# Performance work log

Measured on AMD Instinct MI355X. Metric: run time of the kernel, lower is better.

Reference implementation:

```python
import jax, jax.numpy as jnp
import numpy as np

NH = 8          # attention heads
TEMP = 2.0      # gumbel temperature


def _gumbel_softmax_hard(logits, key, temperature):
    # hard=True straight-through gumbel softmax (module is in eval mode)
    g = jax.random.gumbel(key, logits.shape, logits.dtype)
    y = jax.nn.softmax((logits + g) / temperature, axis=-1)
    y_hard = jax.nn.one_hot(jnp.argmax(y, axis=-1), logits.shape[-1], dtype=y.dtype)
    return y_hard - jax.lax.stop_gradient(y) + y


def _experts(x, w1, w2, w3):
    # SwiGLU FFN over all experts at once: x [T,C], w1/w3 [E,H,C], w2 [E,C,H] -> [T,E,C]
    h = jax.nn.silu(jnp.einsum('tc,ehc->teh', x, w1)) * jnp.einsum('tc,ehc->teh', x, w3)
    return jnp.einsum('teh,ech->tec', h, w2)


def _mha(q_in, kv_in, in_w, in_b, out_w, out_b):
    C = q_in.shape[-1]
    hd = C // NH
    q = q_in @ in_w[:C].T + in_b[:C]
    k = kv_in @ in_w[C:2 * C].T + in_b[C:2 * C]
    v = kv_in @ in_w[2 * C:].T + in_b[2 * C:]
    B, Tq, _ = q.shape
    Tk = k.shape[1]
    q = q.reshape(B, Tq, NH, hd)
    k = k.reshape(B, Tk, NH, hd)
    v = v.reshape(B, Tk, NH, hd)
    scale = jnp.asarray(1.0 / np.sqrt(hd), q.dtype)
    att = jax.nn.softmax(jnp.einsum('bqhd,bkhd->bhqk', q, k) * scale, axis=-1)
    o = jnp.einsum('bhqk,bkhd->bqhd', att, v).reshape(B, Tq, C)
    return o @ out_w.T + out_b


def setup_inputs() -> dict:
    key = jax.random.key(0)
    ks = jax.random.split(key, 20)
    B, T, S, C, E, H = 2, 2048, 77, 1024, 4, 2816
    p = lambda k, sh: jax.random.normal(k, sh, jnp.float32) * 0.02
    return {
        'x': jax.random.normal(ks[0], (B, T, C), jnp.float32),
        'time': jax.random.normal(ks[1], (B,), jnp.float32),
        'caption': jax.random.normal(ks[2], (B, S, C), jnp.float32),
        'language': jax.random.randint(ks[3], (B,), 0, 9),
        'lang_embed': p(ks[4], (9, C)),
        'lang_gate_w': p(ks[5], (E, C)),
        'lang_gate_b': jnp.zeros((E,), jnp.float32),
        'lang_w1': p(ks[6], (E, H, C)),
        'lang_w2': p(ks[7], (E, C, H)),
        'lang_w3': p(ks[8], (E, H, C)),
        'in_proj_w': p(ks[9], (3 * C, C)),
        'in_proj_b': jnp.zeros((3 * C,), jnp.float32),
        'out_proj_w': p(ks[10], (C, C)),
        'out_proj_b': jnp.zeros((C,), jnp.float32),
        'cap_gate_w': p(ks[11], (E, C)),
        'cap_gate_b': jnp.zeros((E,), jnp.float32),
        'cap_w1': p(ks[12], (E, H, C)),
        'cap_w2': p(ks[13], (E, C, H)),
        'cap_w3': p(ks[14], (E, H, C)),
    }


def reference(x, time, caption, language, lang_embed, lang_gate_w, lang_gate_b,
              lang_w1, lang_w2, lang_w3, in_proj_w, in_proj_b, out_proj_w, out_proj_b,
              cap_gate_w, cap_gate_b, cap_w1, cap_w2, cap_w3):
    B, T, C = x.shape
    x_flat = x.reshape(-1, C)                                   # [B*T, C]

    # language gating (one logit vector per batch element, repeated over T tokens)
    lang_emb = lang_embed[language]                             # [B, C]
    lang_logits = lang_emb @ lang_gate_w.T + lang_gate_b        # [B, E]
    lang_probs = _gumbel_softmax_hard(lang_logits, jax.random.key(1), TEMP)
    lang_probs = jnp.repeat(lang_probs, T, axis=0)              # [B*T, E]

    lang_outputs = _experts(x_flat, lang_w1, lang_w2, lang_w3)  # [B*T, E, C]
    first_out = (lang_outputs * lang_probs[:, :, None]).sum(axis=1)  # [B*T, C]
    first_reshaped = first_out.reshape(B, T, C)

    # cross attention against caption, then per-token caption gating
    cross = _mha(first_reshaped, caption, in_proj_w, in_proj_b, out_proj_w, out_proj_b)
    cross_flat = cross.reshape(-1, C)
    cap_logits = cross_flat @ cap_gate_w.T + cap_gate_b         # [B*T, E]
    cap_probs = _gumbel_softmax_hard(cap_logits, jax.random.key(2), TEMP)

    cap_outputs = _experts(first_out, cap_w1, cap_w2, cap_w3)   # [B*T, E, C]
    second_out = (cap_outputs * cap_probs[:, :, None]).sum(axis=1)

    total_out = (first_out + second_out).reshape(B, T, C)

    all_probs = jnp.concatenate([lang_probs, cap_probs], axis=1)  # [B*T, 2E]
    expert_usage = all_probs.mean(axis=0)
    loss = (expert_usage * jnp.log(expert_usage + 1e-10)).sum()
    return total_out, loss
```

## Files before the change

### kernel.cpp

```cpp
#include <hip/hip_runtime.h>
#include <stdint.h>

#define B_ 2
#define T_ 2048
#define S_ 77
#define C_ 1024
#define E_ 4
#define H_ 2816
#define NH_ 8
#define HD_ 128
#define N_ (B_*T_)
#define MAXGB (N_/128 + E_)
#define MAXGB2 (N_/256 + E_)
#define PEsz ((size_t)H_*C_)
#define CC_ ((size_t)C_*C_)

typedef _Float16 h8 __attribute__((ext_vector_type(8)));
typedef _Float16 h4 __attribute__((ext_vector_type(4)));
typedef float f4 __attribute__((ext_vector_type(4)));

__device__ __forceinline__ void gload16(const void* g, void* l){
  __builtin_amdgcn_global_load_lds((const __attribute__((address_space(1))) void*)g,
                                   (__attribute__((address_space(3))) void*)l, 16, 0, 0);
}

__device__ __forceinline__ void xcd_swizzle_cm(int& bx, int& by){
  int nx = gridDim.x, ny = gridDim.y;
  int nwg = nx*ny;
  int wg = by*nx + bx;
  int q = nwg >> 3, r = nwg & 7;
  int xcd = wg & 7, idx = wg >> 3;
  int s = (xcd < r ? xcd*(q+1) : r*(q+1) + (xcd-r)*q) + idx;
  bx = s / ny; by = s % ny;
}

__device__ __forceinline__ uint32_t rotl32(uint32_t v, int r){ return (v<<r)|(v>>(32-r)); }
__device__ __forceinline__ void threefry2x32(uint32_t k0, uint32_t k1,
                                             uint32_t x, uint32_t y,
                                             uint32_t& o0, uint32_t& o1){
  uint32_t k2 = k0 ^ k1 ^ 0x1BD11BDAu;
  x += k0; y += k1;
#define TFR(r) { x += y; y = rotl32(y, r); y ^= x; }
  TFR(13) TFR(15) TFR(26) TFR(6)   x += k1; y += k2 + 1u;
  TFR(17) TFR(29) TFR(16) TFR(24)  x += k2; y += k0 + 2u;
  TFR(13) TFR(15) TFR(26) TFR(6)   x += k0; y += k1 + 3u;
  TFR(17) TFR(29) TFR(16) TFR(24)  x += k1; y += k2 + 4u;
  TFR(13) TFR(15) TFR(26) TFR(6)   x += k2; y += k0 + 5u;
#undef TFR
  o0 = x; o1 = y;
}
__device__ __forceinline__ float gumbel_from_bits(uint32_t bits){
  const float TINY = 1.17549435e-38f;
  float f = __uint_as_float((bits >> 9) | 0x3f800000u) - 1.0f;
  float u = fmaxf(TINY, f + TINY);
  return -logf(-logf(u));
}
__device__ __forceinline__ float jax_gumbel(uint32_t k0, uint32_t k1, uint32_t idx){
  uint32_t a, b;
  threefry2x32(k0, k1, 0u, idx, a, b);
  return gumbel_from_bits(a ^ b);
}

__device__ __forceinline__ void job_split(const float* __restrict__ s,
    _Float16* __restrict__ hi, _Float16* __restrict__ lo, long n4, int b0, int nb){
  for (long i = (long)b0*256 + threadIdx.x; i < n4; i += (long)nb*256){
    float4 v = ((const float4*)s)[i];
    h4 h, L;
    h[0]=(_Float16)v.x; h[1]=(_Float16)v.y; h[2]=(_Float16)v.z; h[3]=(_Float16)v.w;
    L[0]=(_Float16)(v.x-(float)h[0]); L[1]=(_Float16)(v.y-(float)h[1]);
    L[2]=(_Float16)(v.z-(float)h[2]); L[3]=(_Float16)(v.w-(float)h[3]);
    ((h4*)hi)[i] = h; ((h4*)lo)[i] = L;
  }
}
__device__ __forceinline__ void job_plain(const float* __restrict__ s,
    _Float16* __restrict__ d, long n4, int b0, int nb){
  for (long i = (long)b0*256 + threadIdx.x; i < n4; i += (long)nb*256){
    float4 v = ((const float4*)s)[i];
    h4 h;
    h[0]=(_Float16)v.x; h[1]=(_Float16)v.y; h[2]=(_Float16)v.z; h[3]=(_Float16)v.w;
    ((h4*)d)[i] = h;
  }
}
__device__ __forceinline__ void job_w13_plain(const float* __restrict__ w1,
    const float* __restrict__ w3, _Float16* __restrict__ dst, int nslot, int b0, int nb){
  const int K8 = C_/8;
  long total = (long)nslot * (2*H_) * K8;
  for (long i = (long)b0*256 + threadIdx.x; i < total; i += (long)nb*256){
    int kv = (int)(i & (K8-1));
    long rs = i >> 7;
    int r  = (int)(rs % (2*H_));
    int slot = (int)(rs / (2*H_));
    int gg = r >> 5, o = r & 31;
    const float* src = ((o<16)? w1 : w3) + (size_t)slot*PEsz + (size_t)(16*gg + (o&15))*C_ + kv*8;
    float4 v0 = *(const float4*)src, v1 = *(const float4*)(src+4);
    float vv[8] = {v0.x,v0.y,v0.z,v0.w,v1.x,v1.y,v1.z,v1.w};
    h8 hh;
#pragma unroll
    for (int jj=0;jj<8;++jj) hh[jj] = (_Float16)vv[jj];
    *(h8*)(dst + (size_t)slot*2*PEsz + (size_t)r*C_ + kv*8) = hh;
  }
}
__device__ __forceinline__ void job_w13_split_sel(const float* __restrict__ w1,
    const float* __restrict__ w3, int sel0, int sel1,
    _Float16* __restrict__ hi, _Float16* __restrict__ lo, int b0, int nb){
  const int K8 = C_/8;
  long total = 2L * (2*H_) * K8;
  for (long i = (long)b0*256 + threadIdx.x; i < total; i += (long)nb*256){
    int kv = (int)(i & (K8-1));
    long rs = i >> 7;
    int r  = (int)(rs % (2*H_));
    int slot = (int)(rs / (2*H_));
    int e = slot ? sel1 : sel0;
    int gg = r >> 5, o = r & 31;
    const float* src = ((o<16)? w1 : w3) + (size_t)e*PEsz + (size_t)(16*gg + (o&15))*C_ + kv*8;
    float4 v0 = *(const float4*)src, v1 = *(const float4*)(src+4);
    float vv[8] = {v0.x,v0.y,v0.z,v0.w,v1.x,v1.y,v1.z,v1.w};
    h8 hh, ll;
#pragma unroll
    for (int jj=0;jj<8;++jj){
      hh[jj] = (_Float16)vv[jj];
      ll[jj] = (_Float16)(vv[jj]-(float)hh[jj]);
    }
    size_t dof = (size_t)slot*2*PEsz + (size_t)r*C_ + kv*8;
    *(h8*)(hi + dof) = hh;
    *(h8*)(lo + dof) = ll;
  }
}
__device__ __forceinline__ void job_w2_split_sel(const float* __restrict__ w2,
    int sel0, int sel1, _Float16* __restrict__ hi, _Float16* __restrict__ lo, int b0, int nb){
  long per = (long)(PEsz/4);
  for (long i = (long)b0*256 + threadIdx.x; i < 2*per; i += (long)nb*256){
    int slot = (i >= per) ? 1 : 0;
    long ii = i - (long)slot*per;
    float4 v = ((const float4*)(w2 + (size_t)(slot?sel1:sel0)*PEsz))[ii];
    h4 h, L;
    h[0]=(_Float16)v.x; h[1]=(_Float16)v.y; h[2]=(_Float16)v.z; h[3]=(_Float16)v.w;
    L[0]=(_Float16)(v.x-(float)h[0]); L[1]=(_Float16)(v.y-(float)h[1]);
    L[2]=(_Float16)(v.z-(float)h[2]); L[3]=(_Float16)(v.w-(float)h[3]);
    ((h4*)(hi + (size_t)slot*PEsz))[ii] = h;
    ((h4*)(lo + (size_t)slot*PEsz))[ii] = L;
  }
}
__device__ __forceinline__ void job_foldw(const float* __restrict__ outw,
    const float* __restrict__ capgw, const float* __restrict__ outb,
    float* __restrict__ Wp, float* __restrict__ bp, int b0){
  int e = b0 >> 2;
  int k = ((b0 & 3) << 8) + threadIdx.x;
  const float* cg = capgw + e*C_;
  float acc = 0.f;
  for (int c = 0; c < C_; ++c) acc += cg[c] * outw[(size_t)c*C_ + k];
  Wp[e*C_ + k] = acc;
  if ((b0 & 3) == 0){
    int wv = threadIdx.x >> 6, l = threadIdx.x & 63;
    const float* cg2 = capgw + wv*C_;
    float a2 = 0.f;
    for (int c = l; c < C_; c += 64) a2 += outb[c] * cg2[c];
#pragma unroll
    for (int off = 32; off; off >>= 1) a2 += __shfl_xor(a2, off);
    if (l == 0 && e == 0) bp[wv] = a2;
  }
}

#define CVA_W13 1024
#define CVA_W2  512
#define CVA_X   256
#define CVA_TOT (CVA_W13+CVA_W2+CVA_X)
__global__ __launch_bounds__(256) void convA(
    const float* __restrict__ lang_embed, const float* __restrict__ gate_w,
    const float* __restrict__ gate_b, const int* __restrict__ language,
    const float* __restrict__ w1, const float* __restrict__ w3, const float* __restrict__ w2,
    const float* __restrict__ x,
    _Float16* __restrict__ w13hi, _Float16* __restrict__ w13lo,
    _Float16* __restrict__ w2hi, _Float16* __restrict__ w2lo,
    _Float16* __restrict__ xhi, _Float16* __restrict__ xlo,
    float* __restrict__ langP, int* __restrict__ counts)
{
  __shared__ float lds8[8];
  const int tid = threadIdx.x, w = tid>>6, l = tid&63;
  for (int p = 2*w; p < 2*w+2; ++p){
    int b = p>>2, e = p&3;
    const float* emb = lang_embed + (size_t)language[b]*C_;
    const float* gw  = gate_w + (size_t)e*C_;
    float acc = 0.f;
    for (int c = l; c < C_; c += 64) acc += emb[c]*gw[c];
#pragma unroll
    for (int off = 32; off; off >>= 1) acc += __shfl_xor(acc, off);
    if (l == 0) lds8[p] = acc + gate_b[e];
  }
  __syncthreads();
  int sel[2];
  for (int b = 0; b < 2; ++b){
    float z[4], m = -3.4e38f;
    for (int e = 0; e < 4; ++e){
      float g = jax_gumbel(0u, 1u, (uint32_t)(b*4 + e));
      z[e] = (lds8[b*4 + e] + g) * 0.5f;
      m = fmaxf(m, z[e]);
    }
    float y[4], sum = 0.f;
    for (int e = 0; e < 4; ++e){ y[e] = expf(z[e]-m); sum += y[e]; }
    for (int e = 0; e < 4; ++e) y[e] = y[e] / sum;
    int best = 0; float bv = y[0];
    for (int e = 1; e < 4; ++e) if (y[e] > bv){ bv = y[e]; best = e; }
    sel[b] = best;
    if (blockIdx.x == 0 && tid == 0){
      for (int e = 0; e < 4; ++e)
        langP[b*4 + e] = ((e == best) ? 1.0f : 0.0f) - y[e] + y[e];
    }
  }
  if (blockIdx.x == 0 && tid == 0){
    for (int e = 0; e < 4; ++e) counts[e] = 0;
  }
  int bid = blockIdx.x;
  if (bid < CVA_W13)                 job_w13_split_sel(w1, w3, sel[0], sel[1], w13hi, w13lo, bid, CVA_W13);
  else if (bid < CVA_W13+CVA_W2)     job_w2_split_sel(w2, sel[0], sel[1], w2hi, w2lo, bid-CVA_W13, CVA_W2);
  else                               job_split(x, xhi, xlo, (long)((size_t)N_*C_/4), bid-CVA_W13-CVA_W2, CVA_X);
}

__global__ __launch_bounds__(512,2) void gemm_gate_split(
    const _Float16* __restrict__ Ahi, const _Float16* __restrict__ Alo,
    const _Float16* __restrict__ Bhi, const _Float16* __restrict__ Blo,
    _Float16* __restrict__ Hhi, _Float16* __restrict__ Hlo)
{
  __shared__ __align__(16) char smem[147456];
  const int tid = threadIdx.x, w = tid>>6, l = tid&63;
  const int lm = l&15, g = l>>4;
  const int wm = w>>1, wn = w&1;
  int bx = blockIdx.x, by = blockIdx.y;
  xcd_swizzle_cm(bx, by);
  const int n0 = bx<<7;
  const int m0 = by<<8;
  const size_t eoff = (m0 >= T_) ? (size_t)2*PEsz : 0;

  const _Float16* srcA[4]; const _Float16* srcB[2];
#pragma unroll
  for (int jj=0;jj<4;++jj){
    int c = jj*512 + tid, r = c>>3, s = c&7;
    int st = s ^ (r&7);
    srcA[jj] = (st<4 ? Ahi : Alo) + (size_t)(m0 + r)*C_ + ((st&3)<<3);
  }
#pragma unroll
  for (int jj=0;jj<2;++jj){
    int c = jj*512 + tid, r = c>>3, s = c&7;
    int st = s ^ (r&7);
    srcB[jj] = (st<4 ? Bhi : Blo) + eoff + (size_t)(n0 + r)*C_ + ((st&3)<<3);
  }

#define STGF(ts, bi) { \
    int k0 = (ts)<<5; \
    char* db = smem + (bi)*49152; \
    _Pragma("unroll") \
    for (int jj=0;jj<4;++jj) gload16(srcA[jj]+k0, db + (jj*512 + w*64)*16); \
    _Pragma("unroll") \
    for (int jj=0;jj<2;++jj) gload16(srcB[jj]+k0, db + 32768 + (jj*512 + w*64)*16); \
  }

  const int shi = (g ^ (lm&7)) << 4;
  int aoff[4], boff[4];
#pragma unroll
  for (int i=0;i<4;++i){
    aoff[i] = ((wm*64 + i*16 + lm)<<7) + shi;
    boff[i] = 32768 + ((wn*64 + i*16 + lm)<<7) + shi;
  }

  f4 acc[4][4] = {};
  const int nt = C_/32;
  STGF(0,0) STGF(1,1)
  for (int t=0; t<nt; ++t){
    const int bi = t%3;
    const bool ds = (t+2 < nt);
    const int k2 = (t+2)<<5;
    char* db2 = smem + ((t+2)%3)*49152;
    if (t+1 < nt) { asm volatile("s_waitcnt vmcnt(6)" ::: "memory"); }
    else          { asm volatile("s_waitcnt vmcnt(0)" ::: "memory"); }
    __builtin_amdgcn_s_barrier();
    asm volatile("" ::: "memory");
    const char* base = smem + bi*49152;
    if (ds){
      gload16(srcA[0]+k2, db2 + (0*512 + w*64)*16);
      gload16(srcA[1]+k2, db2 + (1*512 + w*64)*16);
    }
    h8 ah[4], bh[4];
#pragma unroll
    for (int i=0;i<4;++i){ ah[i] = *(const h8*)(base + aoff[i]); bh[i] = *(const h8*)(base + boff[i]); }
    __builtin_amdgcn_s_setprio(1);
#pragma unroll
    for (int mi=0;mi<4;++mi)
#pragma unroll
      for (int ni=0;ni<4;++ni)
        acc[mi][ni] = __builtin_amdgcn_mfma_f32_16x16x32_f16(ah[mi], bh[ni], acc[mi][ni],0,0,0);
    __builtin_amdgcn_s_setprio(0);
    if (ds){
      gload16(srcA[2]+k2, db2 + (2*512 + w*64)*16);
      gload16(srcA[3]+k2, db2 + (3*512 + w*64)*16);
    }
    h8 bl[4];
#pragma unroll
    for (int i=0;i<4;++i) bl[i] = *(const h8*)(base + (boff[i]^64));
    __builtin_amdgcn_s_setprio(1);
#pragma unroll
    for (int mi=0;mi<4;++mi)
#pragma unroll
      for (int ni=0;ni<4;++ni)
        acc[mi][ni] = __builtin_amdgcn_mfma_f32_16x16x32_f16(ah[mi], bl[ni], acc[mi][ni],0,0,0);
    __builtin_amdgcn_s_setprio(0);
    if (ds){
      gload16(srcB[0]+k2, db2 + 32768 + (0*512 + w*64)*16);
      gload16(srcB[1]+k2, db2 + 32768 + (1*512 + w*64)*16);
    }
    h8 al[4];
#pragma unroll
    for (int i=0;i<4;++i) al[i] = *(const h8*)(base + (aoff[i]^64));
    __builtin_amdgcn_s_setprio(1);
#pragma unroll
    for (int mi=0;mi<4;++mi)
#pragma unroll
      for (int ni=0;ni<4;++ni)
        acc[mi][ni] = __builtin_amdgcn_mfma_f32_16x16x32_f16(al[mi], bh[ni], acc[mi][ni],0,0,0);
    __builtin_amdgcn_s_setprio(0);
    asm volatile("" ::: "memory");
  }
#undef STGF

#pragma unroll
  for (int mi=0;mi<4;++mi){
#pragma unroll
    for (int p=0;p<2;++p){
      int hc = ((n0 + wn*64)>>1) + p*16 + lm;
#pragma unroll
      for (int j=0;j<4;++j){
        int rl = wm*64 + mi*16 + (g<<2) + j;
        float s1 = acc[mi][2*p][j], s3 = acc[mi][2*p+1][j];
        float hval = s1/(1.f+expf(-s1))*s3;
        size_t row = (size_t)(m0 + rl);
        _Float16 hh = (_Float16)hval;
        Hhi[row*H_ + hc] = hh;
        Hlo[row*H_ + hc] = (_Float16)(hval - (float)hh);
      }
    }
  }
}

__global__ __launch_bounds__(512,2) void gemm_gate_plain(
    const _Float16* __restrict__ A, const _Float16* __restrict__ Bw,
    _Float16* __restrict__ Hout,
    const int* __restrict__ bmap_e, const int* __restrict__ bmap_s,
    const int* __restrict__ offs, const int* __restrict__ perm)
{
  __shared__ __align__(16) char smem[147456];
  const int tid = threadIdx.x, w = tid>>6, l = tid&63;
  const int lm = l&15, g = l>>4;
  const int wm = w>>1, wn = w&1;
  int bx = blockIdx.x, by = blockIdx.y;
  xcd_swizzle_cm(bx, by);
  const int e = bmap_e[by]; if (e<0) return;
  const int m0 = bmap_s[by];
  int v = offs[e+1]-m0; const int valid = v>256?256:v;
  const size_t eoff = (size_t)e*2*PEsz;
  const int n0 = bx<<7;

  const _Float16* srcA[4]; const _Float16* srcB[2];
#pragma unroll
  for (int jj=0;jj<4;++jj){
    int c = jj*512 + tid, r = c>>3, s = c&7;
    int st = s ^ (r&7);
    int ia = m0 + r; ia = (ia<N_) ? ia : (N_-1);
    srcA[jj] = A + (size_t)perm[ia]*C_ + (st<<3);
  }
#pragma unroll
  for (int jj=0;jj<2;++jj){
    int c = jj*512 + tid, r = c>>3, s = c&7;
    int st = s ^ (r&7);
    srcB[jj] = Bw + eoff + (size_t)(n0 + r)*C_ + (st<<3);
  }

#define STGF(ts, bi) { \
    int k0 = (ts)<<6; \
    char* db = smem + (bi)*49152; \
    _Pragma("unroll") \
    for (int jj=0;jj<4;++jj) gload16(srcA[jj]+k0, db + (jj*512 + w*64)*16); \
    _Pragma("unroll") \
    for (int jj=0;jj<2;++jj) gload16(srcB[jj]+k0, db + 32768 + (jj*512 + w*64)*16); \
  }

  const int shi = (g ^ (lm&7)) << 4;
  int aoff[4], boff[4];
#pragma unroll
  for (int i=0;i<4;++i){
    aoff[i] = ((wm*64 + i*16 + lm)<<7) + shi;
    boff[i] = 32768 + ((wn*64 + i*16 + lm)<<7) + shi;
  }

  f4 acc[4][4] = {};
  const int nt = C_/64;
  STGF(0,0) STGF(1,1)
  for (int t=0; t<nt; ++t){
    const int bi = t%3;
    const bool ds = (t+2 < nt);
    const int k2 = (t+2)<<6;
    char* db2 = smem + ((t+2)%3)*49152;
    if (t+1 < nt) { asm volatile("s_waitcnt vmcnt(6)" ::: "memory"); }
    else          { asm volatile("s_waitcnt vmcnt(0)" ::: "memory"); }
    __builtin_amdgcn_s_barrier();
    asm volatile("" ::: "memory");
    const char* base = smem + bi*49152;
#pragma unroll
    for (int kk=0;kk<2;++kk){
      if (ds){
        if (kk == 0){
          gload16(srcA[0]+k2, db2 + (0*512 + w*64)*16);
          gload16(srcA[1]+k2, db2 + (1*512 + w*64)*16);
          gload16(srcA[2]+k2, db2 + (2*512 + w*64)*16);
        } else {
          gload16(srcA[3]+k2, db2 + (3*512 + w*64)*16);
          gload16(srcB[0]+k2, db2 + 32768 + (0*512 + w*64)*16);
          gload16(srcB[1]+k2, db2 + 32768 + (1*512 + w*64)*16);
        }
      }
      h8 af[4], bf[4];
      const int x = kk<<6;
#pragma unroll
      for (int i=0;i<4;++i){ af[i] = *(const h8*)(base + (aoff[i]^x)); bf[i] = *(const h8*)(base + (boff[i]^x)); }
      __builtin_amdgcn_s_setprio(1);
#pragma unroll
      for (int mi=0;mi<4;++mi)
#pragma unroll
        for (int ni=0;ni<4;++ni)
          acc[mi][ni] = __builtin_amdgcn_mfma_f32_16x16x32_f16(af[mi], bf[ni], acc[mi][ni],0,0,0);
      __builtin_amdgcn_s_setprio(0);
    }
    asm volatile("" ::: "memory");
  }
#undef STGF

#pragma unroll
  for (int mi=0;mi<4;++mi){
#pragma unroll
    for (int p=0;p<2;++p){
      int hc = ((n0 + wn*64)>>1) + p*16 + lm;
#pragma unroll
      for (int j=0;j<4;++j){
        int rl = wm*64 + mi*16 + (g<<2) + j;
        if (rl >= valid) continue;
        float s1 = acc[mi][2*p][j], s3 = acc[mi][2*p+1][j];
        Hout[(size_t)(m0 + rl)*H_ + hc] = (_Float16)(s1/(1.f+expf(-s1))*s3);
      }
    }
  }
}

template<int EPI, int NSEG, int EXPM>
__device__ __forceinline__ void gemm8_body(
    char* smem,
    const _Float16* __restrict__ A0, const _Float16* __restrict__ A1,
    const _Float16* __restrict__ B0, const _Float16* __restrict__ B1,
    const float* __restrict__ bias, float* __restrict__ Cf32,
    _Float16* __restrict__ O0, _Float16* __restrict__ O1,
    const int* __restrict__ bmap_e, const int* __restrict__ bmap_s,
    const int* __restrict__ offs, const int* __restrict__ perm,
    int M, int K, int Nw, size_t bstride_e, int bx, int by)
{
  const int tid = threadIdx.x, w = tid>>6, l = tid&63;
  const int lm = l&15, g = l>>4;
  const int wm = w>>1, wn = w&1;
  const int n0 = bx<<7;
  int m0, valid = 128; size_t eoff = 0;
  if constexpr (EXPM==3){
    int e = bmap_e[by]; if (e<0) return;
    m0 = bmap_s[by];
    int v = offs[e+1]-m0; valid = v>128?128:v;
    eoff = (size_t)e*bstride_e;
  } else {
    m0 = by<<7;
    if constexpr (EXPM==1) eoff = (m0>=T_) ? bstride_e : 0;
  }
  const int cAe = (((tid&7) ^ ((tid>>3)&7)) << 3);
  size_t rbA[4], rbB[4];
#pragma unroll
  for (int j=0;j<4;++j){
    int r = (j<<5) + (tid>>3);
    int ia = m0 + r;
    if constexpr (EXPM==3){ ia = (ia < N_) ? ia : (N_-1); }
    else { if (ia > M-1) ia = M-1; }
    rbA[j] = (size_t)ia*K + cAe;
    rbB[j] = eoff + (size_t)(n0+r)*K + cAe;
  }
  const int tps = K>>6, nt = NSEG*tps;

#define STAGE8(tt, cc) { \
    int sg = 0; \
    if constexpr (NSEG==3){ sg = ((tt)>=2*tps) ? 2 : (((tt)>=tps)?1:0); } \
    const _Float16* Asrc = (sg==1) ? A1 : A0; \
    const _Float16* Bsrc = (sg==2) ? B1 : B0; \
    int kk0 = ((tt) - sg*tps)<<6; \
    char* db = smem + (cc)*32768 + w*1024; \
    _Pragma("unroll") \
    for (int j=0;j<4;++j) gload16(Asrc + rbA[j] + kk0, db + j*4096); \
    _Pragma("unroll") \
    for (int j=0;j<4;++j) gload16(Bsrc + rbB[j] + kk0, db + 16384 + j*4096); \
  }

  int aoff[2][4], boff[2][4];
#pragma unroll
  for (int kk=0;kk<2;++kk){
#pragma unroll
    for (int i=0;i<4;++i){
      int ra = wm*64 + i*16 + lm;
      aoff[kk][i] = (ra<<7) + (((kk<<6)+(g<<4)) ^ ((ra&7)<<4));
      int rb = wn*64 + i*16 + lm;
      boff[kk][i] = (rb<<7) + (((kk<<6)+(g<<4)) ^ ((rb&7)<<4));
    }
  }

  f4 acc[4][4] = {};
  STAGE8(0, 0)
  for (int t=0; t<nt; ++t){
    const int c = t&1;
    if (t+1 < nt){
      STAGE8(t+1, c^1)
      asm volatile("s_waitcnt vmcnt(8)" ::: "memory");
    } else {
      asm volatile("s_waitcnt vmcnt(0)" ::: "memory");
    }
    __builtin_amdgcn_s_barrier();
    const char* Ab = smem + c*32768;
    const char* Bb = Ab + 16384;
#pragma unroll
    for (int kk=0;kk<2;++kk){
      h8 af[4], bf[4];
#pragma unroll
      for (int i=0;i<4;++i){
        af[i] = *(const h8*)(Ab + aoff[kk][i]);
        bf[i] = *(const h8*)(Bb + boff[kk][i]);
      }
      __builtin_amdgcn_s_setprio(1);
#pragma unroll
      for (int mi=0;mi<4;++mi)
#pragma unroll
        for (int ni=0;ni<4;++ni)
          acc[mi][ni] = __builtin_amdgcn_mfma_f32_16x16x32_f16(af[mi], bf[ni], acc[mi][ni],0,0,0);
      __builtin_amdgcn_s_setprio(0);
      __builtin_amdgcn_s_barrier();
    }
  }

#pragma unroll
  for (int mi=0;mi<4;++mi){
    const int rl0 = wm*64 + mi*16 + (g<<2);
#pragma unroll
    for (int ni=0;ni<4;++ni){
      int col = n0 + wn*64 + ni*16 + lm;
#pragma unroll
      for (int j=0;j<4;++j){
        int rl = rl0 + j;
        float vv = acc[mi][ni][j];
        if constexpr (EPI==1){
          int grow = m0 + rl;
          if (grow < M){
            float vb = vv + (bias ? bias[col] : 0.f);
            _Float16 hh = (_Float16)vb;
            O0[(size_t)grow*Nw + col] = hh;
            O1[(size_t)grow*Nw + col] = (_Float16)(vb - (float)hh);
          }
        } else {
          if (rl < valid){
            int orig = perm[m0 + rl];
            size_t o = (size_t)orig*C_ + col;
            Cf32[o] = (float)O0[o] + (float)O1[o] + vv;
          }
        }
      }
    }
  }
#undef STAGE8
}

template<int EPI, int NSEG, int EXPM>
__global__ __launch_bounds__(256,2) void gemm8(
    const _Float16* __restrict__ A0, const _Float16* __restrict__ A1,
    const _Float16* __restrict__ B0, const _Float16* __restrict__ B1,
    const float* __restrict__ bias, float* __restrict__ Cf32,
    _Float16* __restrict__ O0, _Float16* __restrict__ O1,
    const int* __restrict__ bmap_e, const int* __restrict__ bmap_s,
    const int* __restrict__ offs, const int* __restrict__ perm,
    int M, int K, int Nw, size_t bstride_e)
{
  __shared__ __align__(16) char smem[65536];
  int bx = blockIdx.x, by = blockIdx.y;
  xcd_swizzle_cm(bx, by);
  gemm8_body<EPI,NSEG,EXPM>(smem, A0,A1,B0,B1,bias,Cf32,O0,O1,
                            bmap_e,bmap_s,offs,perm,M,K,Nw,bstride_e,bx,by);
}

__global__ __launch_bounds__(256,2) void ffn1_out_fused(
    const _Float16* __restrict__ Hbh, const _Float16* __restrict__ Hbl,
    const _Float16* __restrict__ w2hi, const _Float16* __restrict__ w2lo,
    _Float16* __restrict__ Fh, _Float16* __restrict__ Fl,
    const float* __restrict__ in_w,
    const float* __restrict__ cap_w1, const float* __restrict__ cap_w3,
    const float* __restrict__ caption,
    _Float16* __restrict__ inwh, _Float16* __restrict__ inwl,
    _Float16* __restrict__ capw13,
    _Float16* __restrict__ caph, _Float16* __restrict__ capl)
{
  __shared__ __align__(16) char smem[65536];
  int id = blockIdx.x;
  if (id < 256){
    gemm8_body<1,3,1>(smem, Hbh, Hbl, w2hi, w2lo, nullptr, nullptr, Fh, Fl,
                      nullptr,nullptr,nullptr,nullptr, N_, H_, C_, PEsz, id&7, id>>3);
  } else {
    int cid = id - 256;
    if (cid < 352)      job_w13_plain(cap_w1, cap_w3, capw13, 4, cid, 352);
    else if (cid < 496) job_split(in_w, inwh, inwl, (long)(3*CC_/4), cid-352, 144);
    else                job_split(caption, caph, capl, (long)((size_t)B_*S_*C_/4), cid-496, 16);
  }
}

__global__ __launch_bounds__(256,2) void gemm_qkv(
    const _Float16* __restrict__ Fh, const _Float16* __restrict__ Fl,
    const _Float16* __restrict__ caph, const _Float16* __restrict__ capl,
    const _Float16* __restrict__ inwh, const _Float16* __restrict__ inwl,
    const float* __restrict__ in_b,
    _Float16* __restrict__ Qh, _Float16* __restrict__ Ql,
    _Float16* __restrict__ KVh, _Float16* __restrict__ KVl,
    const float* __restrict__ out_w, const float* __restrict__ cap_gw,
    const float* __restrict__ out_b, float* __restrict__ Wp, float* __restrict__ bp)
{
  __shared__ __align__(16) char smem[65536];
  int id = blockIdx.x;
  if (id < 256){
    gemm8_body<1,3,0>(smem, Fh, Fl, inwh, inwl, in_b, nullptr, Qh, Ql,
                      nullptr,nullptr,nullptr,nullptr, N_, C_, C_, 0, id&7, id>>3);
  } else if (id < 288){
    int cid = id - 256;
    gemm8_body<1,3,0>(smem, caph, capl, inwh + CC_, inwl + CC_, in_b + C_,
                      nullptr, KVh, KVl, nullptr,nullptr,nullptr,nullptr,
                      B_*S_, C_, 2*C_, 0, cid & 15, cid >> 4);
  } else {
    job_foldw(out_w, cap_gw, out_b, Wp, bp, id-288);
  }
}

#define SP5 5
#define KSTR 136
#define VSTR 104
__global__ __launch_bounds__(256) void attn_fused(
    const _Float16* __restrict__ Qh, const _Float16* __restrict__ Ql,
    const _Float16* __restrict__ KVh, const _Float16* __restrict__ KVl,
    _Float16* __restrict__ AOh, _Float16* __restrict__ AOl,
    const float* __restrict__ cap_w2, _Float16* __restrict__ capw2f)
{
  __shared__ __align__(16) _Float16 Usm[2*128*VSTR];
  __shared__ __align__(16) _Float16 Psm[2*64*VSTR];
  int id = blockIdx.x;
  if (id >= 512){ job_plain(cap_w2, capw2f, (long)(4*PEsz/4), id-512, 128); return; }
  _Float16* Kh_s = Usm;
  _Float16* Kl_s = Usm + 128*VSTR;
  _Float16* VTh  = Usm;
  _Float16* VTl  = Usm + 128*VSTR;
  _Float16* Ph   = Psm;
  _Float16* Pl   = Psm + 64*VSTR;

  const int tid = threadIdx.x;
  const int w = tid>>6, l = tid&63, lm = l&15, g = l>>4;
  const int b = id >> 8, h = (id >> 5) & 7, q0 = (id & 31) << 6;
  const float scale = 0.08838834764831845f;

  for (int i = tid; i < 64*VSTR; i += 256) ((uint32_t*)Psm)[i] = 0;
  {
    int oct = tid & 15, s0 = tid >> 4;
    for (int s = s0; s < 80; s += 16){
      h8 vh = {}, vl = {};
      if (s < S_){
        size_t ga = ((size_t)(b*S_ + s))*(2*C_) + h*HD_ + oct*8;
        vh = *(const h8*)(KVh + ga);
        vl = *(const h8*)(KVl + ga);
      }
      *(h8*)(Kh_s + s*KSTR + oct*8) = vh;
      *(h8*)(Kl_s + s*KSTR + oct*8) = vl;
    }
  }
  h8 qh[4], ql[4];
  {
    size_t qrow = (size_t)(b*T_ + q0 + w*16 + lm);
    const _Float16* qph = Qh + qrow*C_ + h*HD_ + g*8;
    const _Float16* qpl = Ql + qrow*C_ + h*HD_ + g*8;
#pragma unroll
    for (int ks=0; ks<4; ++ks){ qh[ks] = *(const h8*)(qph + ks*32); ql[ks] = *(const h8*)(qpl + ks*32); }
  }
  __syncthreads();

  f4 sc[SP5] = {};
#pragma unroll
  for (int ks=0; ks<4; ++ks){
#pragma unroll
    for (int nt=0; nt<SP5; ++nt){
      h8 kh = *(const h8*)(Kh_s + (nt*16+lm)*KSTR + ks*32 + g*8);
      h8 kl = *(const h8*)(Kl_s + (nt*16+lm)*KSTR + ks*32 + g*8);
      sc[nt] = __builtin_amdgcn_mfma_f32_16x16x32_f16(qh[ks], kh, sc[nt],0,0,0);
      sc[nt] = __builtin_amdgcn_mfma_f32_16x16x32_f16(ql[ks], kh, sc[nt],0,0,0);
      sc[nt] = __builtin_amdgcn_mfma_f32_16x16x32_f16(qh[ks], kl, sc[nt],0,0,0);
    }
  }

  float mx[4] = {-3e38f,-3e38f,-3e38f,-3e38f};
#pragma unroll
  for (int nt=0; nt<SP5; ++nt){
    bool valid = (nt*16+lm) < S_;
#pragma unroll
    for (int j=0;j<4;++j){
      float v = valid ? sc[nt][j]*scale : -3e38f;
      sc[nt][j] = v;
      mx[j] = fmaxf(mx[j], v);
    }
  }
#pragma unroll
  for (int off=1; off<16; off<<=1){
#pragma unroll
    for (int j=0;j<4;++j) mx[j] = fmaxf(mx[j], __shfl_xor(mx[j], off));
  }
  float sm[4] = {0,0,0,0};
#pragma unroll
  for (int nt=0; nt<SP5; ++nt){
    bool valid = (nt*16+lm) < S_;
#pragma unroll
    for (int j=0;j<4;++j){
      float p = valid ? expf(sc[nt][j]-mx[j]) : 0.f;
      sc[nt][j] = p; sm[j] += p;
    }
  }
#pragma unroll
  for (int off=1; off<16; off<<=1){
#pragma unroll
    for (int j=0;j<4;++j) sm[j] += __shfl_xor(sm[j], off);
  }
#pragma unroll
  for (int nt=0; nt<SP5; ++nt){
#pragma unroll
// ... 82 lines not shown
      lg[e] = p + bp[e] + gb[e];
    }
    if (lane == 0){
      float z[E_], m = -3.4e38f;
      for (int e = 0; e < E_; ++e){
        float gmb = jax_gumbel(0u, 2u, (uint32_t)(row*E_ + e));
        z[e] = (lg[e] + gmb) * 0.5f;
        m = fmaxf(m, z[e]);
      }
      float y[E_], sum = 0.f;
      for (int e = 0; e < E_; ++e){ y[e] = expf(z[e] - m); sum += y[e]; }
      for (int e = 0; e < E_; ++e) y[e] = y[e] / sum;
      int best = 0; float bv = y[0];
      for (int e = 1; e < E_; ++e) if (y[e] > bv){ bv = y[e]; best = e; }
      cap_sel[row] = best;
      atomicAdd(&counts[best], 1);
      for (int e = 0; e < E_; ++e)
        capP[(size_t)row*E_ + e] = ((e == best) ? 1.0f : 0.0f) - y[e] + y[e];
    }
  }
}

__global__ __launch_bounds__(256) void finalize(
    const int* __restrict__ counts, const int* __restrict__ cap_sel,
    int* __restrict__ offs,
    int* __restrict__ bmap_e, int* __restrict__ bmap_s,
    int* __restrict__ bmap_e2, int* __restrict__ bmap_s2,
    int* __restrict__ perm,
    const float* __restrict__ capP, const float* __restrict__ langP,
    float* __restrict__ out_loss)
{
  __shared__ int loffs[5];
  __shared__ int lcur[4];
  __shared__ float red[4][256];
  int tid = threadIdx.x;
  if (blockIdx.x == 0){
    if (tid == 0){
      loffs[0] = 0;
      for (int e = 0; e < E_; ++e){ loffs[e+1] = loffs[e] + counts[e]; lcur[e] = loffs[e]; }
      for (int e = 0; e < E_+1; ++e) offs[e] = loffs[e];
      int idx = 0;
      for (int e = 0; e < E_; ++e)
        for (int s = loffs[e]; s < loffs[e+1]; s += 128){ bmap_e[idx] = e; bmap_s[idx] = s; ++idx; }
      for (; idx < MAXGB; ++idx) bmap_e[idx] = -1;
      int idx2 = 0;
      for (int e = 0; e < E_; ++e)
        for (int s = loffs[e]; s < loffs[e+1]; s += 256){ bmap_e2[idx2] = e; bmap_s2[idx2] = s; ++idx2; }
      for (; idx2 < MAXGB2; ++idx2) bmap_e2[idx2] = -1;
    }
    __syncthreads();
    for (int row = tid; row < N_; row += 256){
      int e = cap_sel[row];
      int pos = atomicAdd(&lcur[e], 1);
      perm[pos] = row;
    }
  } else {
    float p0=0.f, p1=0.f, p2=0.f, p3=0.f;
    for (int r = tid; r < N_; r += 256){
      const float* p = capP + (size_t)r*E_;
      p0 += p[0]; p1 += p[1]; p2 += p[2]; p3 += p[3];
    }
    red[0][tid]=p0; red[1][tid]=p1; red[2][tid]=p2; red[3][tid]=p3;
    __syncthreads();
    for (int s = 128; s > 0; s >>= 1){
      if (tid < s){
        red[0][tid]+=red[0][tid+s]; red[1][tid]+=red[1][tid+s];
        red[2][tid]+=red[2][tid+s]; red[3][tid]+=red[3][tid+s];
      }
      __syncthreads();
    }
    if (tid == 0){
      float loss = 0.f;
      for (int e = 0; e < E_; ++e){
        float ul = (langP[e] + langP[E_ + e]) * 0.5f;
        loss += ul * logf(ul + 1e-10f);
      }
      for (int e = 0; e < E_; ++e){
        float uc = red[e][0] * (1.0f / N_);
        loss += uc * logf(uc + 1e-10f);
      }
      out_loss[0] = loss;
    }
  }
}

extern "C" void kernel_launch(void* const* d_in, const int* in_sizes, int n_in,
                              void* d_out, int out_size, void* d_ws, size_t ws_size,
                              hipStream_t stream)
{
  const float* x          = (const float*)d_in[0];
  const float* caption    = (const float*)d_in[2];
  const int*   language   = (const int*)  d_in[3];
  const float* lang_embed = (const float*)d_in[4];
  const float* lang_gw    = (const float*)d_in[5];
  const float* lang_gb    = (const float*)d_in[6];
  const float* lang_w1    = (const float*)d_in[7];
  const float* lang_w2    = (const float*)d_in[8];
  const float* lang_w3    = (const float*)d_in[9];
  const float* in_w       = (const float*)d_in[10];
  const float* in_b       = (const float*)d_in[11];
  const float* out_w      = (const float*)d_in[12];
  const float* out_b      = (const float*)d_in[13];
  const float* cap_gw     = (const float*)d_in[14];
  const float* cap_gb     = (const float*)d_in[15];
  const float* cap_w1     = (const float*)d_in[16];
  const float* cap_w2     = (const float*)d_in[17];
  const float* cap_w3     = (const float*)d_in[18];
  float* out = (float*)d_out;

  const size_t NC = (size_t)N_*C_;
  const size_t NHe = (size_t)N_*H_;
  const size_t KVel = (size_t)B_*S_*2*C_;
  const size_t CAPel = (size_t)B_*S_*C_;

  char* base = (char*)d_ws;
  size_t cur = 0;
  auto alloc = [&](size_t bytes)->char*{
    char* p = base + cur;
    cur += (bytes + 255) & ~(size_t)255;
    return p;
  };
  _Float16* Qh = (_Float16*)alloc(NC*2);
  _Float16* Ql = (_Float16*)alloc(NC*2);
  char* kvreg = alloc(KVel*4);
  _Float16* KVh = (_Float16*)kvreg;
  _Float16* KVl = KVh + KVel;
  float* capP   = (float*)alloc((size_t)N_*E_*4);
  float* langP  = (float*)alloc(64);
  float* Wp     = (float*)alloc(E_*C_*4);
  float* bp     = (float*)alloc(64);
  int* cap_sel  = (int*)alloc(N_*4);
  int* counts   = (int*)alloc(64);
  int* offs     = (int*)alloc(64);
  int* bmap_e   = (int*)alloc(MAXGB*4);
  int* bmap_s   = (int*)alloc(MAXGB*4);
  int* bmap_e2  = (int*)alloc(MAXGB2*4);
  int* bmap_s2  = (int*)alloc(MAXGB2*4);
  int* perm     = (int*)alloc(N_*4);
  _Float16* xAO_hi = (_Float16*)alloc(NC*2);
  _Float16* xAO_lo = (_Float16*)alloc(NC*2);
  _Float16* cap_hi = (_Float16*)alloc(CAPel*2);
  _Float16* cap_lo = (_Float16*)alloc(CAPel*2);
  _Float16* Hb_hi  = (_Float16*)alloc(NHe*2);
  _Float16* Hb_lo  = (_Float16*)alloc(NHe*2);
  _Float16* F_hi   = (_Float16*)alloc(NC*2);
  _Float16* F_lo   = (_Float16*)alloc(NC*2);
  _Float16* Wreg = (_Float16*)alloc(2*( (size_t)3*CC_*2 + CC_*2 + 3*4*PEsz ));
  _Float16* w13hi = Wreg;
  _Float16* w13lo = Wreg + 4*PEsz;
  _Float16* w2hi  = Wreg + 8*PEsz;
  _Float16* w2lo  = Wreg + 10*PEsz;
  _Float16* capw13f = Wreg;
  _Float16* capw2f  = Wreg + 8*PEsz;
  _Float16* inw_hi  = Wreg + 12*PEsz;
  _Float16* inw_lo  = inw_hi + 3*CC_;

  convA<<<CVA_TOT, 256, 0, stream>>>(
      lang_embed, lang_gw, lang_gb, language,
      lang_w1, lang_w3, lang_w2, x,
      w13hi, w13lo, w2hi, w2lo, xAO_hi, xAO_lo, langP, counts);

  gemm_gate_split<<<dim3((2*H_)/128, N_/256), 512, 0, stream>>>(
      xAO_hi, xAO_lo, w13hi, w13lo, Hb_hi, Hb_lo);

  ffn1_out_fused<<<768, 256, 0, stream>>>(
      Hb_hi, Hb_lo, w2hi, w2lo, F_hi, F_lo,
      in_w, cap_w1, cap_w3, caption,
      inw_hi, inw_lo, capw13f, cap_hi, cap_lo);

  gemm_qkv<<<304, 256, 0, stream>>>(
      F_hi, F_lo, cap_hi, cap_lo, inw_hi, inw_lo, in_b,
      Qh, Ql, KVh, KVl, out_w, cap_gw, out_b, Wp, bp);

  attn_fused<<<640, 256, 0, stream>>>(Qh, Ql, KVh, KVl, xAO_hi, xAO_lo, cap_w2, capw2f);

  cap_gate<<<N_/8, 256, 0, stream>>>(xAO_hi, xAO_lo, Wp, bp, cap_gb, cap_sel, capP, counts);

  finalize<<<2, 256, 0, stream>>>(counts, cap_sel, offs, bmap_e, bmap_s,
                                  bmap_e2, bmap_s2, perm, capP, langP, out + NC);

  _Float16* H2 = Hb_hi;
  gemm_gate_plain<<<dim3((2*H_)/128, MAXGB2), 512, 0, stream>>>(
      F_hi, capw13f, H2, bmap_e2, bmap_s2, offs, perm);

  gemm8<2,1,3><<<dim3(C_/128, MAXGB), 256, 0, stream>>>(
      H2, nullptr, capw2f, nullptr, nullptr, out, F_hi, F_lo,
      bmap_e, bmap_s, offs, perm, N_, H_, C_, PEsz);
}
```

Measured before the change: 640.0 us.

## Restructure conversion jobs, add triple-buffered GEMM pipeline, relocate cap weight buffers

```diff
diff --git a/kernel.cpp b/kernel.cpp
--- a/kernel.cpp
+++ b/kernel.cpp
@@ -22,16 +22,6 @@
 __device__ __forceinline__ void gload16(const void* g, void* l){
   __builtin_amdgcn_global_load_lds((const __attribute__((address_space(1))) void*)g,
                                    (__attribute__((address_space(3))) void*)l, 16, 0, 0);
-}
-
-__device__ __forceinline__ void xcd_swizzle_cm(int& bx, int& by){
-  int nx = gridDim.x, ny = gridDim.y;
-  int nwg = nx*ny;
-  int wg = by*nx + bx;
-  int q = nwg >> 3, r = nwg & 7;
-  int xcd = wg & 7, idx = wg >> 3;
-  int s = (xcd < r ? xcd*(q+1) : r*(q+1) + (xcd-r)*q) + idx;
-  bx = s / ny; by = s % ny;
 }
 
 __device__ __forceinline__ uint32_t rotl32(uint32_t v, int r){ return (v<<r)|(v>>(32-r)); }
@@ -62,8 +52,8 @@
 }
 
 __device__ __forceinline__ void job_split(const float* __restrict__ s,
-    _Float16* __restrict__ hi, _Float16* __restrict__ lo, long n4, int b0, int nb){
-  for (long i = (long)b0*256 + threadIdx.x; i < n4; i += (long)nb*256){
+    _Float16* __restrict__ hi, _Float16* __restrict__ lo, long n4, long gtid, long gstride){
+  for (long i = gtid; i < n4; i += gstride){
     float4 v = ((const float4*)s)[i];
     h4 h, L;
     h[0]=(_Float16)v.x; h[1]=(_Float16)v.y; h[2]=(_Float16)v.z; h[3]=(_Float16)v.w;
@@ -73,8 +63,8 @@
   }
 }
 __device__ __forceinline__ void job_plain(const float* __restrict__ s,
-    _Float16* __restrict__ d, long n4, int b0, int nb){
-  for (long i = (long)b0*256 + threadIdx.x; i < n4; i += (long)nb*256){
+    _Float16* __restrict__ d, long n4, long gtid, long gstride){
+  for (long i = gtid; i < n4; i += gstride){
     float4 v = ((const float4*)s)[i];
     h4 h;
     h[0]=(_Float16)v.x; h[1]=(_Float16)v.y; h[2]=(_Float16)v.z; h[3]=(_Float16)v.w;
@@ -82,10 +72,10 @@
   }
 }
 __device__ __forceinline__ void job_w13_plain(const float* __restrict__ w1,
-    const float* __restrict__ w3, _Float16* __restrict__ dst, int nslot, int b0, int nb){
+    const float* __restrict__ w3, _Float16* __restrict__ dst, int nslot, long gtid, long gstride){
   const int K8 = C_/8;
   long total = (long)nslot * (2*H_) * K8;
-  for (long i = (long)b0*256 + threadIdx.x; i < total; i += (long)nb*256){
+  for (long i = gtid; i < total; i += gstride){
     int kv = (int)(i & (K8-1));
     long rs = i >> 7;
     int r  = (int)(rs % (2*H_));
@@ -102,10 +92,10 @@
 }
 __device__ __forceinline__ void job_w13_split_sel(const float* __restrict__ w1,
     const float* __restrict__ w3, int sel0, int sel1,
-    _Float16* __restrict__ hi, _Float16* __restrict__ lo, int b0, int nb){
+    _Float16* __restrict__ hi, _Float16* __restrict__ lo, long gtid, long gstride){
   const int K8 = C_/8;
   long total = 2L * (2*H_) * K8;
-  for (long i = (long)b0*256 + threadIdx.x; i < total; i += (long)nb*256){
+  for (long i = gtid; i < total; i += gstride){
     int kv = (int)(i & (K8-1));
     long rs = i >> 7;
     int r  = (int)(rs % (2*H_));
@@ -127,9 +117,9 @@
   }
 }
 __device__ __forceinline__ void job_w2_split_sel(const float* __restrict__ w2,
-    int sel0, int sel1, _Float16* __restrict__ hi, _Float16* __restrict__ lo, int b0, int nb){
+    int sel0, int sel1, _Float16* __restrict__ hi, _Float16* __restrict__ lo, long gtid, long gstride){
   long per = (long)(PEsz/4);
-  for (long i = (long)b0*256 + threadIdx.x; i < 2*per; i += (long)nb*256){
+  for (long i = gtid; i < 2*per; i += gstride){
     int slot = (i >= per) ? 1 : 0;
     long ii = i - (long)slot*per;
     float4 v = ((const float4*)(w2 + (size_t)(slot?sel1:sel0)*PEsz))[ii];
@@ -211,22 +201,48 @@
     for (int e = 0; e < 4; ++e) counts[e] = 0;
   }
   int bid = blockIdx.x;
-  if (bid < CVA_W13)                 job_w13_split_sel(w1, w3, sel[0], sel[1], w13hi, w13lo, bid, CVA_W13);
-  else if (bid < CVA_W13+CVA_W2)     job_w2_split_sel(w2, sel[0], sel[1], w2hi, w2lo, bid-CVA_W13, CVA_W2);
-  else                               job_split(x, xhi, xlo, (long)((size_t)N_*C_/4), bid-CVA_W13-CVA_W2, CVA_X);
-}
-
-__global__ __launch_bounds__(512,2) void gemm_gate_split(
+  if (bid < CVA_W13)
+    job_w13_split_sel(w1, w3, sel[0], sel[1], w13hi, w13lo,
+                      (long)bid*256 + tid, (long)CVA_W13*256);
+  else if (bid < CVA_W13+CVA_W2)
+    job_w2_split_sel(w2, sel[0], sel[1], w2hi, w2lo,
+                     (long)(bid-CVA_W13)*256 + tid, (long)CVA_W2*256);
+  else
+    job_split(x, xhi, xlo, (long)((size_t)N_*C_/4),
+              (long)(bid-CVA_W13-CVA_W2)*256 + tid, (long)CVA_X*256);
+}
+
+#define GS_GEMM 704
+#define GS_RID  640
+__global__ __launch_bounds__(512) void gemm_gate_split(
     const _Float16* __restrict__ Ahi, const _Float16* __restrict__ Alo,
     const _Float16* __restrict__ Bhi, const _Float16* __restrict__ Blo,
-    _Float16* __restrict__ Hhi, _Float16* __restrict__ Hlo)
+    _Float16* __restrict__ Hhi, _Float16* __restrict__ Hlo,
+    const float* __restrict__ cap_w1, const float* __restrict__ cap_w3,
+    const float* __restrict__ in_w, const float* __restrict__ caption,
+    const float* __restrict__ cap_w2,
+    _Float16* __restrict__ capw13, _Float16* __restrict__ inwh, _Float16* __restrict__ inwl,
+    _Float16* __restrict__ caph, _Float16* __restrict__ capl, _Float16* __restrict__ capw2f)
 {
   __shared__ __align__(16) char smem[147456];
-  const int tid = threadIdx.x, w = tid>>6, l = tid&63;
+  const int tid = threadIdx.x;
+  int bid = blockIdx.x;
+  if (bid >= GS_GEMM){
+    int rid = bid - GS_GEMM;
+    if (rid < 352)      job_w13_plain(cap_w1, cap_w3, capw13, 4, (long)rid*512 + tid, 352L*512);
+    else if (rid < 496) job_split(in_w, inwh, inwl, (long)(3*CC_/4), (long)(rid-352)*512 + tid, 144L*512);
+    else if (rid < 512) job_split(caption, caph, capl, (long)((size_t)B_*S_*C_/4), (long)(rid-496)*512 + tid, 16L*512);
+    else                job_plain(cap_w2, capw2f, (long)(4*PEsz/4), (long)(rid-512)*512 + tid, 128L*512);
+    return;
+  }
+  {
+    int xcd = bid & 7, idx = bid >> 3;
+    bid = xcd*88 + idx;
+  }
+  const int bx = bid / 16, by = bid % 16;
+  const int w = tid>>6, l = tid&63;
   const int lm = l&15, g = l>>4;
   const int wm = w>>1, wn = w&1;
-  int bx = blockIdx.x, by = blockIdx.y;
-  xcd_swizzle_cm(bx, by);
   const int n0 = bx<<7;
   const int m0 = by<<8;
   const size_t eoff = (m0 >= T_) ? (size_t)2*PEsz : 0;
@@ -340,7 +356,7 @@
   }
 }
 
-__global__ __launch_bounds__(512,2) void gemm_gate_plain(
+__global__ __launch_bounds__(512) void gemm_gate_plain(
     const _Float16* __restrict__ A, const _Float16* __restrict__ Bw,
     _Float16* __restrict__ Hout,
     const int* __restrict__ bmap_e, const int* __restrict__ bmap_s,
@@ -351,7 +367,15 @@
   const int lm = l&15, g = l>>4;
   const int wm = w>>1, wn = w&1;
   int bx = blockIdx.x, by = blockIdx.y;
-  xcd_swizzle_cm(bx, by);
+  {
+    int nx = gridDim.x, ny = gridDim.y;
+    int nwg = nx*ny;
+    int wg = by*nx + bx;
+    int q = nwg >> 3, r = nwg & 7;
+    int xcd = wg & 7, idx = wg >> 3;
+    int s = (xcd < r ? xcd*(q+1) : r*(q+1) + (xcd-r)*q) + idx;
+    bx = s / ny; by = s % ny;
+  }
   const int e = bmap_e[by]; if (e<0) return;
   const int m0 = bmap_s[by];
   int v = offs[e+1]-m0; const int valid = v>256?256:v;
@@ -448,7 +472,7 @@
   }
 }
 
-template<int EPI, int NSEG, int EXPM>
+template<int EPI, int NSEG, int EXPM, int NBUF>
 __device__ __forceinline__ void gemm8_body(
     char* smem,
     const _Float16* __restrict__ A0, const _Float16* __restrict__ A1,
@@ -486,15 +510,22 @@
   }
   const int tps = K>>6, nt = NSEG*tps;
 
-#define STAGE8(tt, cc) { \
+#define SEGDEC(tt, kkv, Asrcv, Bsrcv) \
     int sg = 0; \
     if constexpr (NSEG==3){ sg = ((tt)>=2*tps) ? 2 : (((tt)>=tps)?1:0); } \
-    const _Float16* Asrc = (sg==1) ? A1 : A0; \
-    const _Float16* Bsrc = (sg==2) ? B1 : B0; \
-    int kk0 = ((tt) - sg*tps)<<6; \
+    const _Float16* Asrcv = (sg==1) ? A1 : A0; \
+    const _Float16* Bsrcv = (sg==2) ? B1 : B0; \
+    int kkv = ((tt) - sg*tps)<<6;
+
+#define STG_A(tt, cc) { \
+    SEGDEC(tt, kk0, Asrc, Bsrc) (void)Bsrc; \
     char* db = smem + (cc)*32768 + w*1024; \
     _Pragma("unroll") \
     for (int j=0;j<4;++j) gload16(Asrc + rbA[j] + kk0, db + j*4096); \
+  }
+#define STG_B(tt, cc) { \
+    SEGDEC(tt, kk0, Asrc, Bsrc) (void)Asrc; \
+    char* db = smem + (cc)*32768 + w*1024; \
     _Pragma("unroll") \
     for (int j=0;j<4;++j) gload16(Bsrc + rbB[j] + kk0, db + 16384 + j*4096); \
   }
@@ -512,25 +543,30 @@
   }
 
   f4 acc[4][4] = {};
-  STAGE8(0, 0)
+  STG_A(0,0) STG_B(0,0)
+  if constexpr (NBUF==3){ STG_A(1,1) STG_B(1,1) }
   for (int t=0; t<nt; ++t){
-    const int c = t&1;
+    const int rb = t % NBUF;
+    const int ts = t + NBUF - 1;
+    const bool ds = ts < nt;
+    const int wbuf = ts % NBUF;
     if (t+1 < nt){
-      STAGE8(t+1, c^1)
-      asm volatile("s_waitcnt vmcnt(8)" ::: "memory");
+      if constexpr (NBUF==3) asm volatile("s_waitcnt vmcnt(8)" ::: "memory");
+      else                   asm volatile("s_waitcnt vmcnt(0)" ::: "memory");
     } else {
       asm volatile("s_waitcnt vmcnt(0)" ::: "memory");
     }
     __builtin_amdgcn_s_barrier();
-    const char* Ab = smem + c*32768;
+    asm volatile("" ::: "memory");
+    const char* Ab = smem + rb*32768;
     const char* Bb = Ab + 16384;
-#pragma unroll
-    for (int kk=0;kk<2;++kk){
+    if (ds) STG_A(ts, wbuf)
+    {
       h8 af[4], bf[4];
 #pragma unroll
       for (int i=0;i<4;++i){
-        af[i] = *(const h8*)(Ab + aoff[kk][i]);
-        bf[i] = *(const h8*)(Bb + boff[kk][i]);
+        af[i] = *(const h8*)(Ab + aoff[0][i]);
+        bf[i] = *(const h8*)(Bb + boff[0][i]);
       }
       __builtin_amdgcn_s_setprio(1);
 #pragma unroll
@@ -539,8 +575,24 @@
         for (int ni=0;ni<4;++ni)
           acc[mi][ni] = __builtin_amdgcn_mfma_f32_16x16x32_f16(af[mi], bf[ni], acc[mi][ni],0,0,0);
       __builtin_amdgcn_s_setprio(0);
-      __builtin_amdgcn_s_barrier();
-    }
+    }
+    if (ds) STG_B(ts, wbuf)
+    {
+      h8 af[4], bf[4];
+#pragma unroll
+      for (int i=0;i<4;++i){
+        af[i] = *(const h8*)(Ab + aoff[1][i]);
+        bf[i] = *(const h8*)(Bb + boff[1][i]);
+      }
+      __builtin_amdgcn_s_setprio(1);
+#pragma unroll
+      for (int mi=0;mi<4;++mi)
+#pragma unroll
+        for (int ni=0;ni<4;++ni)
+          acc[mi][ni] = __builtin_amdgcn_mfma_f32_16x16x32_f16(af[mi], bf[ni], acc[mi][ni],0,0,0);
+      __builtin_amdgcn_s_setprio(0);
+    }
+    asm volatile("" ::: "memory");
   }
 
 #pragma unroll
@@ -571,51 +623,23 @@
       }
     }
   }
-#undef STAGE8
-}
-
-template<int EPI, int NSEG, int EXPM>
-__global__ __launch_bounds__(256,2) void gemm8(
-    const _Float16* __restrict__ A0, const _Float16* __restrict__ A1,
-    const _Float16* __restrict__ B0, const _Float16* __restrict__ B1,
-    const float* __restrict__ bias, float* __restrict__ Cf32,
-    _Float16* __restrict__ O0, _Float16* __restrict__ O1,
-    const int* __restrict__ bmap_e, const int* __restrict__ bmap_s,
-    const int* __restrict__ offs, const int* __restrict__ perm,
-    int M, int K, int Nw, size_t bstride_e)
-{
-  __shared__ __align__(16) char smem[65536];
-  int bx = blockIdx.x, by = blockIdx.y;
-  xcd_swizzle_cm(bx, by);
-  gemm8_body<EPI,NSEG,EXPM>(smem, A0,A1,B0,B1,bias,Cf32,O0,O1,
-                            bmap_e,bmap_s,offs,perm,M,K,Nw,bstride_e,bx,by);
-}
-
-__global__ __launch_bounds__(256,2) void ffn1_out_fused(
+#undef STG_A
+#undef STG_B
+#undef SEGDEC
+}
+
+__global__ __launch_bounds__(256) void ffn1_out(
     const _Float16* __restrict__ Hbh, const _Float16* __restrict__ Hbl,
     const _Float16* __restrict__ w2hi, const _Float16* __restrict__ w2lo,
-    _Float16* __restrict__ Fh, _Float16* __restrict__ Fl,
-    const float* __restrict__ in_w,
-    const float* __restrict__ cap_w1, const float* __restrict__ cap_w3,
-    const float* __restrict__ caption,
-    _Float16* __restrict__ inwh, _Float16* __restrict__ inwl,
-    _Float16* __restrict__ capw13,
-    _Float16* __restrict__ caph, _Float16* __restrict__ capl)
+    _Float16* __restrict__ Fh, _Float16* __restrict__ Fl)
 {
-  __shared__ __align__(16) char smem[65536];
+  __shared__ __align__(16) char smem[98304];
   int id = blockIdx.x;
-  if (id < 256){
-    gemm8_body<1,3,1>(smem, Hbh, Hbl, w2hi, w2lo, nullptr, nullptr, Fh, Fl,
+  gemm8_body<1,3,1,3>(smem, Hbh, Hbl, w2hi, w2lo, nullptr, nullptr, Fh, Fl,
                       nullptr,nullptr,nullptr,nullptr, N_, H_, C_, PEsz, id&7, id>>3);
-  } else {
-    int cid = id - 256;
-    if (cid < 352)      job_w13_plain(cap_w1, cap_w3, capw13, 4, cid, 352);
-    else if (cid < 496) job_split(in_w, inwh, inwl, (long)(3*CC_/4), cid-352, 144);
-    else                job_split(caption, caph, capl, (long)((size_t)B_*S_*C_/4), cid-496, 16);
-  }
-}
-
-__global__ __launch_bounds__(256,2) void gemm_qkv(
+}
+
+__global__ __launch_bounds__(256) void gemm_qkv(
     const _Float16* __restrict__ Fh, const _Float16* __restrict__ Fl,
     const _Float16* __restrict__ caph, const _Float16* __restrict__ capl,
     const _Float16* __restrict__ inwh, const _Float16* __restrict__ inwl,
@@ -628,13 +652,13 @@
   __shared__ __align__(16) char smem[65536];
   int id = blockIdx.x;
   if (id < 256){
-    gemm8_body<1,3,0>(smem, Fh, Fl, inwh, inwl, in_b, nullptr, Qh, Ql,
-                      nullptr,nullptr,nullptr,nullptr, N_, C_, C_, 0, id&7, id>>3);
+    gemm8_body<1,3,0,2>(smem, Fh, Fl, inwh, inwl, in_b, nullptr, Qh, Ql,
+                        nullptr,nullptr,nullptr,nullptr, N_, C_, C_, 0, id&7, id>>3);
   } else if (id < 288){
     int cid = id - 256;
-    gemm8_body<1,3,0>(smem, caph, capl, inwh + CC_, inwl + CC_, in_b + C_,
-                      nullptr, KVh, KVl, nullptr,nullptr,nullptr,nullptr,
-                      B_*S_, C_, 2*C_, 0, cid & 15, cid >> 4);
+    gemm8_body<1,3,0,2>(smem, caph, capl, inwh + CC_, inwl + CC_, in_b + C_,
+                        nullptr, KVh, KVl, nullptr,nullptr,nullptr,nullptr,
+                        B_*S_, C_, 2*C_, 0, cid & 15, cid >> 4);
   } else {
     job_foldw(out_w, cap_gw, out_b, Wp, bp, id-288);
   }
@@ -643,16 +667,14 @@
 #define SP5 5
 #define KSTR 136
 #define VSTR 104
-__global__ __launch_bounds__(256) void attn_fused(
+__global__ __launch_bounds__(256) void attn_mfma(
     const _Float16* __restrict__ Qh, const _Float16* __restrict__ Ql,
     const _Float16* __restrict__ KVh, const _Float16* __restrict__ KVl,
-    _Float16* __restrict__ AOh, _Float16* __restrict__ AOl,
-    const float* __restrict__ cap_w2, _Float16* __restrict__ capw2f)
+    _Float16* __restrict__ AOh, _Float16* __restrict__ AOl)
 {
   __shared__ __align__(16) _Float16 Usm[2*128*VSTR];
   __shared__ __align__(16) _Float16 Psm[2*64*VSTR];
   int id = blockIdx.x;
-  if (id >= 512){ job_plain(cap_w2, capw2f, (long)(4*PEsz/4), id-512, 128); return; }
   _Float16* Kh_s = Usm;
   _Float16* Kl_s = Usm + 128*VSTR;
   _Float16* VTh  = Usm;
@@ -901,6 +923,29 @@
       out_loss[0] = loss;
     }
   }
+}
+
+__global__ __launch_bounds__(256) void ffn2_out(
+    const _Float16* __restrict__ H2, const _Float16* __restrict__ capw2f,
+    float* __restrict__ out,
+    const _Float16* __restrict__ Fh, const _Float16* __restrict__ Fl,
+    const int* __restrict__ bmap_e, const int* __restrict__ bmap_s,
+    const int* __restrict__ offs, const int* __restrict__ perm)
+{
+  __shared__ __align__(16) char smem[65536];
+  int bx = blockIdx.x, by = blockIdx.y;
+  {
+    int nx = gridDim.x, ny = gridDim.y;
+    int nwg = nx*ny;
+    int wg = by*nx + bx;
+    int q = nwg >> 3, r = nwg & 7;
+    int xcd = wg & 7, idx = wg >> 3;
+    int s = (xcd < r ? xcd*(q+1) : r*(q+1) + (xcd-r)*q) + idx;
+    bx = s / ny; by = s % ny;
+  }
+  gemm8_body<2,1,3,2>(smem, H2, nullptr, capw2f, nullptr, nullptr, out,
+                      (_Float16*)Fh, (_Float16*)Fl,
+                      bmap_e, bmap_s, offs, perm, N_, H_, C_, PEsz, bx, by);
 }
 
 extern "C" void kernel_launch(void* const* d_in, const int* in_sizes, int n_in,
@@ -969,29 +1014,28 @@
   _Float16* w13lo = Wreg + 4*PEsz;
   _Float16* w2hi  = Wreg + 8*PEsz;
   _Float16* w2lo  = Wreg + 10*PEsz;
-  _Float16* capw13f = Wreg;
-  _Float16* capw2f  = Wreg + 8*PEsz;
   _Float16* inw_hi  = Wreg + 12*PEsz;
   _Float16* inw_lo  = inw_hi + 3*CC_;
+  _Float16* capw13f = Wreg + 12*PEsz + 6*CC_;
+  _Float16* capw2f  = capw13f + 8*PEsz;
 
   convA<<<CVA_TOT, 256, 0, stream>>>(
       lang_embed, lang_gw, lang_gb, language,
       lang_w1, lang_w3, lang_w2, x,
       w13hi, w13lo, w2hi, w2lo, xAO_hi, xAO_lo, langP, counts);
 
-  gemm_gate_split<<<dim3((2*H_)/128, N_/256), 512, 0, stream>>>(
-      xAO_hi, xAO_lo, w13hi, w13lo, Hb_hi, Hb_lo);
-
-  ffn1_out_fused<<<768, 256, 0, stream>>>(
-      Hb_hi, Hb_lo, w2hi, w2lo, F_hi, F_lo,
-      in_w, cap_w1, cap_w3, caption,
-      inw_hi, inw_lo, capw13f, cap_hi, cap_lo);
+  gemm_gate_split<<<GS_GEMM + GS_RID, 512, 0, stream>>>(
+      xAO_hi, xAO_lo, w13hi, w13lo, Hb_hi, Hb_lo,
+      cap_w1, cap_w3, in_w, caption, cap_w2,
+      capw13f, inw_hi, inw_lo, cap_hi, cap_lo, capw2f);
+
+  ffn1_out<<<256, 256, 0, stream>>>(Hb_hi, Hb_lo, w2hi, w2lo, F_hi, F_lo);
 
   gemm_qkv<<<304, 256, 0, stream>>>(
       F_hi, F_lo, cap_hi, cap_lo, inw_hi, inw_lo, in_b,
       Qh, Ql, KVh, KVl, out_w, cap_gw, out_b, Wp, bp);
 
-  attn_fused<<<640, 256, 0, stream>>>(Qh, Ql, KVh, KVl, xAO_hi, xAO_lo, cap_w2, capw2f);
+  attn_mfma<<<512, 256, 0, stream>>>(Qh, Ql, KVh, KVl, xAO_hi, xAO_lo);
 
   cap_gate<<<N_/8, 256, 0, stream>>>(xAO_hi, xAO_lo, Wp, bp, cap_gb, cap_sel, capP, counts);
 
@@ -1002,7 +1046,6 @@
   gemm_gate_plain<<<dim3((2*H_)/128, MAXGB2), 512, 0, stream>>>(
       F_hi, capw13f, H2, bmap_e2, bmap_s2, offs, perm);
 
-  gemm8<2,1,3><<<dim3(C_/128, MAXGB), 256, 0, stream>>>(
-      H2, nullptr, capw2f, nullptr, nullptr, out, F_hi, F_lo,
-      bmap_e, bmap_s, offs, perm, N_, H_, C_, PEsz);
-}
+  ffn2_out<<<dim3(C_/128, MAXGB), 256, 0, stream>>>(
+      H2, capw2f, out, F_hi, F_lo, bmap_e, bmap_s, offs, perm);
+}
```

Result: no change. 647.8 us (+1.2%).
